# Kernel optimization log

Measured on AMD Instinct MI355X. Metric: run time of the kernel, lower is better.

Reference implementation:

```python
import jax, jax.numpy as jnp
import numpy as np

N, C_IN, EDGE = 32, 64, 64
C_OUT, KH, KW = 128, 3, 3
STRIDE, PAD = 1, 1


def setup_inputs() -> dict:
    key = jax.random.key(0)
    k1, k2, k3 = jax.random.split(key, 3)
    s = 2.4 / (C_IN * KW * KH)  # lecun_init bound from the module
    x = jax.random.normal(k1, (N, C_IN, EDGE, EDGE), dtype=jnp.float32)
    weight = jax.random.uniform(k2, (C_IN * KW * KH, C_OUT), dtype=jnp.float32, minval=-s, maxval=s)
    bias = jax.random.uniform(k3, (1, C_OUT, 1, 1), dtype=jnp.float32, minval=-s, maxval=s)
    return {"input": x, "weight": weight, "bias": bias}


def reference(input, weight, bias):
    # torch.nn.Unfold orders the patch axis as c*kh*kw + i*kw + j, so the
    # (C_in*kh*kw, C_out) weight reshapes to (C_in, kh, kw, C_out).
    k = weight.reshape(C_IN, KH, KW, C_OUT)
    k = jnp.transpose(k, (3, 0, 1, 2))  # OIHW
    out = jax.lax.conv_general_dilated(
        input, k,
        window_strides=(STRIDE, STRIDE),
        padding=[(PAD, PAD), (PAD, PAD)],
        dimension_numbers=("NCHW", "OIHW", "NCHW"),
    )
    return out + bias
```

## Files before the change

kernel.cpp:

```cpp
#include <hip/hip_runtime.h>
#include <cstdint>
#include <cstddef>

#define CIN   64
#define CH_   64
#define CW_   64
#define COUT  128

typedef short  s16x8  __attribute__((ext_vector_type(8)));
typedef float  f32x16 __attribute__((ext_vector_type(16)));

__device__ __forceinline__ unsigned short f32_to_bf16(float f) {
    unsigned int u = __builtin_bit_cast(unsigned int, f);
    u = u + 0x7FFFu + ((u >> 16) & 1u);
    return (unsigned short)(u >> 16);
}

__global__ __launch_bounds__(256) void wconv_prep(const float* __restrict__ wgt,
                                                  unsigned short* __restrict__ wdst) {
    int tid = blockIdx.x * 256 + threadIdx.x;
    if (tid >= 576 * 128) return;
    int row = tid >> 7;
    int co  = tid & 127;
    int c   = row / 9;
    int tap = row - c * 9;
    float f = wgt[tid];
    wdst[((tap * 8 + (c >> 3)) * 128 + co) * 8 + (c & 7)] = f32_to_bf16(f);
}

#define XROW 1072
__global__ __launch_bounds__(256, 4) void conv_mfma(
    const float* __restrict__ x,
    const float* __restrict__ bias,
    const unsigned short* __restrict__ wbf,
    float* __restrict__ out)
{
    __shared__ __align__(16) unsigned char lds_x[32 * XROW];

    const int tid  = threadIdx.x;
    const int lane = tid & 63;
    const int wid  = tid >> 6;
    const int hi   = lane >> 5;
    const int l31  = lane & 31;
    const int wm   = wid >> 1;
    const int wn   = wid & 1;

    const int bid = blockIdx.x;
    const int swz = (bid & 7) * 128 + (bid >> 3);
    const int n   = swz >> 5;
    const int hb  = swz & 31;
    const int h0  = hb * 2;

    const float* xn = x + (size_t)n * CIN * CH_ * CW_;

    #pragma unroll
    for (int it = 0; it < 2; ++it) {
        const int idx = tid + it * 256;
        const int g  = idx & 15;
        const int ck = (idx >> 4) & 7;
        const int r  = idx >> 7;
        const int grow = h0 - 1 + r;
        s16x8 pk[4] = {};
        if (grow >= 0 && grow < CH_) {
            #pragma unroll
            for (int e = 0; e < 8; ++e) {
                const float4 v = *(const float4*)(xn + ((size_t)(ck * 8 + e) * CH_ + grow) * CW_ + 4 * g);
                pk[0][e] = (short)f32_to_bf16(v.x);
                pk[1][e] = (short)f32_to_bf16(v.y);
                pk[2][e] = (short)f32_to_bf16(v.z);
                pk[3][e] = (short)f32_to_bf16(v.w);
            }
        }
        unsigned char* rowp = lds_x + (r * 8 + ck) * XROW;
        #pragma unroll
        for (int q = 0; q < 4; ++q)
            *(s16x8*)(rowp + (4 * g + 1 + q) * 16) = pk[q];
    }
    if (tid < 64) {
        const int t  = (tid & 1) ? 65 : 0;
        const int ck = (tid >> 1) & 7;
        const int r  = tid >> 4;
        s16x8 z = {};
        *(s16x8*)(lds_x + (r * 8 + ck) * XROW + t * 16) = z;
    }
    __syncthreads();

    f32x16 acc00 = {}, acc01 = {}, acc10 = {}, acc11 = {};
    const s16x8* wB = (const s16x8*)wbf;
    const int bbase = wn * 64 + l31 + hi * 128;

#define LOADB(dst, tap) do {                                                   \
    _Pragma("unroll") for (int cc = 0; cc < 4; ++cc) {                         \
        dst[2*cc]   = wB[(tap) * 1024 + cc * 256 + bbase];                     \
        dst[2*cc+1] = wB[(tap) * 1024 + cc * 256 + bbase + 32];                \
    } } while (0)

#define COMP(bb, tap) do {                                                     \
    const int i_ = (tap) / 3, j_ = (tap) % 3;                                  \
    const unsigned aCol = (unsigned)(l31 + j_) * 16;                           \
    _Pragma("unroll") for (int cc = 0; cc < 4; ++cc) {                         \
        const unsigned rr = (unsigned)((wm + i_) * 8 + cc * 2 + hi);           \
        const unsigned aO0 = rr * XROW + aCol;                                 \
        s16x8 a0 = *(const s16x8*)(lds_x + aO0);                               \
        s16x8 a1 = *(const s16x8*)(lds_x + aO0 + 32 * 16);                     \
        acc00 = __builtin_amdgcn_mfma_f32_32x32x16_bf16(a0, bb[2*cc],   acc00, 0, 0, 0); \
        acc01 = __builtin_amdgcn_mfma_f32_32x32x16_bf16(a0, bb[2*cc+1], acc01, 0, 0, 0); \
        acc10 = __builtin_amdgcn_mfma_f32_32x32x16_bf16(a1, bb[2*cc],   acc10, 0, 0, 0); \
        acc11 = __builtin_amdgcn_mfma_f32_32x32x16_bf16(a1, bb[2*cc+1], acc11, 0, 0, 0); \
    } } while (0)

    s16x8 bA[8], bB[8];
    LOADB(bA, 0);
    #pragma unroll
    for (int tt = 0; tt < 4; ++tt) {
        LOADB(bB, 2 * tt + 1);
        COMP(bA, 2 * tt);
        LOADB(bA, 2 * tt + 2);
        COMP(bB, 2 * tt + 1);
    }
    COMP(bA, 8);

    const int h = h0 + wm;
    #pragma unroll
    for (int fn = 0; fn < 2; ++fn) {
        const int co = wn * 64 + fn * 32 + l31;
        const float bv = bias[co];
        float* op = out + (((size_t)n * COUT + co) * CH_ + h) * CW_ + 4 * hi;
        #pragma unroll
        for (int fm = 0; fm < 2; ++fm) {
            const f32x16 a = fn == 0 ? (fm == 0 ? acc00 : acc10)
                                     : (fm == 0 ? acc01 : acc11);
            #pragma unroll
            for (int q = 0; q < 4; ++q) {
                float4 v = make_float4(a[4*q+0] + bv, a[4*q+1] + bv,
                                       a[4*q+2] + bv, a[4*q+3] + bv);
                *(float4*)(op + fm * 32 + 8 * q) = v;
            }
        }
    }
#undef LOADB
#undef COMP
}

__global__ __launch_bounds__(256) void conv_direct_f32(
    const float* __restrict__ x, const float* __restrict__ wgt,
    const float* __restrict__ bias, float* __restrict__ out)
{
    const int w = threadIdx.x, ty = threadIdx.y;
    const int cog = blockIdx.x, h = blockIdx.y, n = blockIdx.z;
    const int co0 = cog * 32 + ty * 8;
    float acc[8];
    #pragma unroll
    for (int k = 0; k < 8; ++k) acc[k] = bias[co0 + k];
    const float* xn = x + (size_t)n * CIN * CH_ * CW_;
    for (int c = 0; c < CIN; ++c) {
        const float* xc = xn + (size_t)c * CH_ * CW_;
        #pragma unroll
        for (int i = 0; i < 3; ++i) {
            const int hh = h - 1 + i;
            if (hh < 0 || hh >= CH_) continue;
            const float* xr = xc + hh * CW_;
            #pragma unroll
            for (int j = 0; j < 3; ++j) {
                const int ww = w - 1 + j;
                const float v = (ww >= 0 && ww < CW_) ? xr[ww] : 0.0f;
                const float* wp = wgt + (size_t)((c * 9 + i * 3 + j) * COUT) + co0;
                const float4 w0 = *reinterpret_cast<const float4*>(wp);
                const float4 w1 = *reinterpret_cast<const float4*>(wp + 4);
                acc[0] += v * w0.x; acc[1] += v * w0.y; acc[2] += v * w0.z; acc[3] += v * w0.w;
                acc[4] += v * w1.x; acc[5] += v * w1.y; acc[6] += v * w1.z; acc[7] += v * w1.w;
            }
        }
    }
    float* op = out + (((size_t)n * COUT + co0) * CH_ + h) * CW_ + w;
    #pragma unroll
    for (int k = 0; k < 8; ++k) op[(size_t)k * CH_ * CW_] = acc[k];
}

extern "C" void kernel_launch(void* const* d_in, const int* in_sizes, int n_in,
                              void* d_out, int out_size, void* d_ws, size_t ws_size,
                              hipStream_t stream) {
    const float* x    = (const float*)d_in[0];
    const float* wgt  = (const float*)d_in[1];
    const float* bias = (const float*)d_in[2];
    float* out        = (float*)d_out;

    if (ws_size >= (size_t)(9 * 8 * 128 * 8) * sizeof(unsigned short)) {
        wconv_prep<<<288, 256, 0, stream>>>(wgt, (unsigned short*)d_ws);
        conv_mfma<<<1024, 256, 0, stream>>>(x, bias, (const unsigned short*)d_ws, out);
    } else {
        conv_direct_f32<<<dim3(4, 64, 32), dim3(64, 4, 1), 0, stream>>>(x, wgt, bias, out);
    }
}
```

Baseline: 114.2 us.

## Enlarge conv tile to four output rows per block with swapped MFMA operands

Each block now computes four output rows instead of two, so each wave holds eight 32x32 accumulators and reuses every weight fragment across four input fragments. The grid is halved, the LDS input tile grows to six rows, and weight preloads are issued before the input staging. MFMA operands are swapped so the accumulator layout maps lanes to width, bias is folded into the accumulator initialisation, and stores become scalar coalesced writes along width. The cost is higher register and LDS use (launch bounds lowered to 2 blocks per SIMD) and fewer blocks to hide latency.

```diff
diff --git a/kernel.cpp b/kernel.cpp
--- a/kernel.cpp
+++ b/kernel.cpp
@@ -29,13 +29,15 @@
 }
 
 #define XROW 1072
-__global__ __launch_bounds__(256, 4) void conv_mfma(
+#define MFMA_SW(d, wf, xf) d = __builtin_amdgcn_mfma_f32_32x32x16_bf16((wf), (xf), (d), 0, 0, 0)
+
+__global__ __launch_bounds__(256, 2) void conv_mfma(
     const float* __restrict__ x,
     const float* __restrict__ bias,
     const unsigned short* __restrict__ wbf,
     float* __restrict__ out)
 {
-    __shared__ __align__(16) unsigned char lds_x[32 * XROW];
+    __shared__ __align__(16) unsigned char lds_x[48 * XROW];
 
     const int tid  = threadIdx.x;
     const int lane = tid & 63;
@@ -46,15 +48,27 @@
     const int wn   = wid & 1;
 
     const int bid = blockIdx.x;
-    const int swz = (bid & 7) * 128 + (bid >> 3);
-    const int n   = swz >> 5;
-    const int hb  = swz & 31;
-    const int h0  = hb * 2;
+    const int swz = (bid & 7) * 64 + (bid >> 3);
+    const int n   = swz >> 4;
+    const int hb  = swz & 15;
+    const int h0  = hb * 4;
+
+    const s16x8* wB = (const s16x8*)wbf;
+    const int bbase = wn * 64 + l31 + hi * 128;
+
+#define LOADB(dst, tap) do {                                                   \
+    _Pragma("unroll") for (int cc = 0; cc < 4; ++cc) {                         \
+        dst[2*cc]   = wB[(tap) * 1024 + cc * 256 + bbase];                     \
+        dst[2*cc+1] = wB[(tap) * 1024 + cc * 256 + bbase + 32];                \
+    } } while (0)
+
+    s16x8 bA[8], bB[8];
+    LOADB(bA, 0);
+    LOADB(bB, 1);
 
     const float* xn = x + (size_t)n * CIN * CH_ * CW_;
-
-    #pragma unroll
-    for (int it = 0; it < 2; ++it) {
+    #pragma unroll
+    for (int it = 0; it < 3; ++it) {
         const int idx = tid + it * 256;
         const int g  = idx & 15;
         const int ck = (idx >> 4) & 7;
@@ -76,7 +90,7 @@
         for (int q = 0; q < 4; ++q)
             *(s16x8*)(rowp + (4 * g + 1 + q) * 16) = pk[q];
     }
-    if (tid < 64) {
+    if (tid < 96) {
         const int t  = (tid & 1) ? 65 : 0;
         const int ck = (tid >> 1) & 7;
         const int r  = tid >> 4;
@@ -85,58 +99,57 @@
     }
     __syncthreads();
 
-    f32x16 acc00 = {}, acc01 = {}, acc10 = {}, acc11 = {};
-    const s16x8* wB = (const s16x8*)wbf;
-    const int bbase = wn * 64 + l31 + hi * 128;
-
-#define LOADB(dst, tap) do {                                                   \
-    _Pragma("unroll") for (int cc = 0; cc < 4; ++cc) {                         \
-        dst[2*cc]   = wB[(tap) * 1024 + cc * 256 + bbase];                     \
-        dst[2*cc+1] = wB[(tap) * 1024 + cc * 256 + bbase + 32];                \
-    } } while (0)
+    f32x16 acc000, acc001, acc010, acc011, acc100, acc101, acc110, acc111;
+    #pragma unroll
+    for (int r = 0; r < 16; ++r) {
+        const int cq = 4 * hi + (r & 3) + 8 * (r >> 2);
+        const float bv0 = bias[wn * 64 + cq];
+        const float bv1 = bias[wn * 64 + 32 + cq];
+        acc000[r] = bv0; acc010[r] = bv0; acc100[r] = bv0; acc110[r] = bv0;
+        acc001[r] = bv1; acc011[r] = bv1; acc101[r] = bv1; acc111[r] = bv1;
+    }
 
 #define COMP(bb, tap) do {                                                     \
     const int i_ = (tap) / 3, j_ = (tap) % 3;                                  \
     const unsigned aCol = (unsigned)(l31 + j_) * 16;                           \
     _Pragma("unroll") for (int cc = 0; cc < 4; ++cc) {                         \
-        const unsigned rr = (unsigned)((wm + i_) * 8 + cc * 2 + hi);           \
-        const unsigned aO0 = rr * XROW + aCol;                                 \
-        s16x8 a0 = *(const s16x8*)(lds_x + aO0);                               \
-        s16x8 a1 = *(const s16x8*)(lds_x + aO0 + 32 * 16);                     \
-        acc00 = __builtin_amdgcn_mfma_f32_32x32x16_bf16(a0, bb[2*cc],   acc00, 0, 0, 0); \
-        acc01 = __builtin_amdgcn_mfma_f32_32x32x16_bf16(a0, bb[2*cc+1], acc01, 0, 0, 0); \
-        acc10 = __builtin_amdgcn_mfma_f32_32x32x16_bf16(a1, bb[2*cc],   acc10, 0, 0, 0); \
-        acc11 = __builtin_amdgcn_mfma_f32_32x32x16_bf16(a1, bb[2*cc+1], acc11, 0, 0, 0); \
+        const unsigned ch = (unsigned)(cc * 2 + hi);                           \
+        const unsigned aO = ((unsigned)(2 * wm + i_) * 8 + ch) * XROW + aCol;  \
+        s16x8 a00 = *(const s16x8*)(lds_x + aO);                               \
+        s16x8 a01 = *(const s16x8*)(lds_x + aO + 512);                         \
+        s16x8 a10 = *(const s16x8*)(lds_x + aO + 8 * XROW);                    \
+        s16x8 a11 = *(const s16x8*)(lds_x + aO + 8 * XROW + 512);              \
+        MFMA_SW(acc000, bb[2*cc],   a00);                                      \
+        MFMA_SW(acc001, bb[2*cc+1], a00);                                      \
+        MFMA_SW(acc010, bb[2*cc],   a01);                                      \
+        MFMA_SW(acc011, bb[2*cc+1], a01);                                      \
+        MFMA_SW(acc100, bb[2*cc],   a10);                                      \
+        MFMA_SW(acc101, bb[2*cc+1], a10);                                      \
+        MFMA_SW(acc110, bb[2*cc],   a11);                                      \
+        MFMA_SW(acc111, bb[2*cc+1], a11);                                      \
     } } while (0)
 
-    s16x8 bA[8], bB[8];
-    LOADB(bA, 0);
-    #pragma unroll
-    for (int tt = 0; tt < 4; ++tt) {
-        LOADB(bB, 2 * tt + 1);
-        COMP(bA, 2 * tt);
-        LOADB(bA, 2 * tt + 2);
-        COMP(bB, 2 * tt + 1);
-    }
+    COMP(bA, 0); LOADB(bA, 2);
+    COMP(bB, 1); LOADB(bB, 3);
+    COMP(bA, 2); LOADB(bA, 4);
+    COMP(bB, 3); LOADB(bB, 5);
+    COMP(bA, 4); LOADB(bA, 6);
+    COMP(bB, 5); LOADB(bB, 7);
+    COMP(bA, 6); LOADB(bA, 8);
+    COMP(bB, 7);
     COMP(bA, 8);
 
-    const int h = h0 + wm;
-    #pragma unroll
-    for (int fn = 0; fn < 2; ++fn) {
-        const int co = wn * 64 + fn * 32 + l31;
-        const float bv = bias[co];
-        float* op = out + (((size_t)n * COUT + co) * CH_ + h) * CW_ + 4 * hi;
-        #pragma unroll
-        for (int fm = 0; fm < 2; ++fm) {
-            const f32x16 a = fn == 0 ? (fm == 0 ? acc00 : acc10)
-                                     : (fm == 0 ? acc01 : acc11);
-            #pragma unroll
-            for (int q = 0; q < 4; ++q) {
-                float4 v = make_float4(a[4*q+0] + bv, a[4*q+1] + bv,
-                                       a[4*q+2] + bv, a[4*q+3] + bv);
-                *(float4*)(op + fm * 32 + 8 * q) = v;
-            }
-        }
+    const int hB = h0 + 2 * wm;
+    float* outn = out + (size_t)n * COUT * (CH_ * CW_);
+    #pragma unroll
+    for (int r = 0; r < 16; ++r) {
+        const int cq = 4 * hi + (r & 3) + 8 * (r >> 2);
+        float* p0 = outn + (size_t)(wn * 64 + cq) * (CH_ * CW_) + hB * CW_ + l31;
+        float* p1 = outn + (size_t)(wn * 64 + 32 + cq) * (CH_ * CW_) + hB * CW_ + l31;
+        p0[0]  = acc000[r];  p0[32]      = acc010[r];
+        p0[64] = acc100[r];  p0[64 + 32] = acc110[r];
+        p1[0]  = acc001[r];  p1[32]      = acc011[r];
+        p1[64] = acc101[r];  p1[64 + 32] = acc111[r];
     }
 #undef LOADB
 #undef COMP
@@ -187,7 +200,7 @@
 
     if (ws_size >= (size_t)(9 * 8 * 128 * 8) * sizeof(unsigned short)) {
         wconv_prep<<<288, 256, 0, stream>>>(wgt, (unsigned short*)d_ws);
-        conv_mfma<<<1024, 256, 0, stream>>>(x, bias, (const unsigned short*)d_ws, out);
+        conv_mfma<<<512, 256, 0, stream>>>(x, bias, (const unsigned short*)d_ws, out);
     } else {
         conv_direct_f32<<<dim3(4, 64, 32), dim3(64, 4, 1), 0, stream>>>(x, wgt, bias, out);
     }
```

Result: no change. 114.0 us (-0.2%).
